# Kernel tuning notes

Hardware: AMD Instinct MI355X
Metric: run time of the kernel (lower is better)

## Reference

```python
import jax, jax.numpy as jnp
import numpy as np

B, S, D = 4, 2048, 1024
E, K, H = 8, 2, 4096


def setup_inputs() -> dict:
    key = jax.random.key(0)
    ks = jax.random.split(key, 8)
    sd = 1.0 / np.sqrt(D)
    sh = 1.0 / np.sqrt(H)
    x = jax.random.normal(ks[0], (B, S, D), dtype=jnp.float32)
    gate_w = jax.random.normal(ks[1], (D, E), dtype=jnp.float32) * sd
    gate_b = jnp.zeros((E,), dtype=jnp.float32)
    w1 = jax.random.normal(ks[2], (E, D, H), dtype=jnp.float32) * sd
    b1 = jnp.zeros((E, H), dtype=jnp.float32)
    w2 = jax.random.normal(ks[3], (E, H, D), dtype=jnp.float32) * sh
    b2 = jnp.zeros((E, D), dtype=jnp.float32)
    return {"x": x, "gate_w": gate_w, "gate_b": gate_b,
            "w1": w1, "b1": b1, "w2": w2, "b2": b2}


def reference(x, gate_w, gate_b, w1, b1, w2, b2):
    # gate logits [B,S,E]
    logits = jnp.einsum('bsd,de->bse', x, gate_w) + gate_b
    # top-k over experts, softmax over the k selected (dim=2), in float32
    weights, selected = jax.lax.top_k(logits, K)            # [B,S,K]
    weights = jax.nn.softmax(weights.astype(jnp.float32), axis=-1).astype(x.dtype)
    out = jnp.zeros_like(x)
    for i in range(E):
        # per-token combine weight for expert i (0 if not routed here)
        w_i = jnp.sum(jnp.where(selected == i, weights, 0.0), axis=-1)  # [B,S]
        h = jax.nn.gelu(jnp.einsum('bsd,dh->bsh', x, w1[i]) + b1[i])    # [B,S,H]
        y = jnp.einsum('bsh,hd->bsd', h, w2[i]) + b2[i]                  # [B,S,D]
        out = out + w_i[..., None] * y
    return out
```

## Files before the change

### kernel.cpp

```cpp
#include <hip/hip_runtime.h>
#include <hip/hip_bf16.h>
#include <stdint.h>

#define T_TOK 8192
#define D_DIM 1024
#define E_NUM 8
#define H_DIM 4096
#define WL_MAX 72

typedef short bf16x8 __attribute__((ext_vector_type(8)));
typedef float f32x4 __attribute__((ext_vector_type(4)));

#define AS1 __attribute__((address_space(1)))
#define AS3 __attribute__((address_space(3)))

__device__ __forceinline__ unsigned short f2b(float f) {
  union { float f; uint32_t u; } v; v.f = f;
  uint32_t r = (v.u + 0x7fffu + ((v.u >> 16) & 1u)) >> 16;
  return (unsigned short)r;
}

__device__ __forceinline__ float gelu_tanh(float x) {
  float u = 0.7978845608028654f * (x + 0.044715f * x * x * x);
  u = fminf(fmaxf(u, -15.f), 15.f);
  float e = __expf(2.f * u);
  float t = (e - 1.f) / (e + 1.f);
  return 0.5f * x * (1.f + t);
}

__device__ __forceinline__ void gload_lds16(const void* g, void* l) {
  __builtin_amdgcn_global_load_lds((const AS1 uint32_t*)g, (AS3 uint32_t*)l, 16, 0, 0);
}

__global__ __launch_bounds__(256) void moe_gate_conv(const float* __restrict__ x,
                                                     const float* __restrict__ gw,
                                                     const float* __restrict__ gb,
                                                     unsigned short* __restrict__ xb,
                                                     int2* __restrict__ sel,
                                                     float2* __restrict__ wts,
                                                     int* __restrict__ meta) {
  int lane = threadIdx.x & 63;
  int t = blockIdx.x * 4 + (threadIdx.x >> 6);
  const float* xr = x + (size_t)t * D_DIM;
  unsigned short* xo = xb + (size_t)t * D_DIM;
  float acc[8];
#pragma unroll
  for (int e = 0; e < 8; e++) acc[e] = 0.f;
#pragma unroll
  for (int i = 0; i < 4; i++) {
    int d0 = lane * 4 + i * 256;
    float4 xv = *(const float4*)(xr + d0);
    ushort4 o;
    o.x = f2b(xv.x); o.y = f2b(xv.y); o.z = f2b(xv.z); o.w = f2b(xv.w);
    *(ushort4*)(xo + d0) = o;
    const float* gp = gw + (size_t)d0 * 8;
    float xs[4] = {xv.x, xv.y, xv.z, xv.w};
#pragma unroll
    for (int j = 0; j < 4; j++) {
#pragma unroll
      for (int e = 0; e < 8; e++) acc[e] += xs[j] * gp[j * 8 + e];
    }
  }
#pragma unroll
  for (int off = 32; off > 0; off >>= 1) {
#pragma unroll
    for (int e = 0; e < 8; e++) acc[e] += __shfl_xor(acc[e], off);
  }
  if (lane == 0) {
    float lg[8];
#pragma unroll
    for (int e = 0; e < 8; e++) lg[e] = acc[e] + gb[e];
    int e0 = 0; float b0 = lg[0];
#pragma unroll
    for (int e = 1; e < 8; e++) if (lg[e] > b0) { b0 = lg[e]; e0 = e; }
    int e1 = -1; float b1v = -1e30f;
#pragma unroll
    for (int e = 0; e < 8; e++) if (e != e0 && lg[e] > b1v) { b1v = lg[e]; e1 = e; }
    float d = __expf(b1v - b0);
    float w0 = 1.f / (1.f + d), w1 = d / (1.f + d);
    sel[t] = make_int2(e0, e1);
    wts[t] = make_float2(w0, w1);
    atomicAdd(&meta[e0], 1);
    atomicAdd(&meta[e1], 1);
  }
}

__global__ __launch_bounds__(256) void moe_transpose(const float* __restrict__ in,
                                                     unsigned short* __restrict__ out,
                                                     int R, int C) {
  int e = blockIdx.z;
  int c0 = blockIdx.x * 64, r0 = blockIdx.y * 64;
  __shared__ float tile[64][65];
  const float* ine = in + (size_t)e * R * C;
  unsigned short* oute = out + (size_t)e * R * C;
  int tr = threadIdx.x >> 2;
  int tc4 = (threadIdx.x & 3) * 16;
#pragma unroll
  for (int p = 0; p < 4; p++) {
    int c = tc4 + p * 4;
    float4 v = *(const float4*)(ine + (size_t)(r0 + tr) * C + c0 + c);
    tile[tr][c] = v.x; tile[tr][c + 1] = v.y; tile[tr][c + 2] = v.z; tile[tr][c + 3] = v.w;
  }
  __syncthreads();
#pragma unroll
  for (int p = 0; p < 4; p++) {
    int rr = tc4 + p * 4;
    ushort4 o;
    o.x = f2b(tile[rr + 0][tr]);
    o.y = f2b(tile[rr + 1][tr]);
    o.z = f2b(tile[rr + 2][tr]);
    o.w = f2b(tile[rr + 3][tr]);
    *(ushort4*)(oute + (size_t)(c0 + tr) * R + r0 + rr) = o;
  }
}

__global__ void moe_scan(int* meta, int2* wl) {
  if (threadIdx.x == 0 && blockIdx.x == 0) {
    int o = 0;
    for (int e = 0; e < 8; e++) { meta[8 + e] = o; meta[20 + e] = o; o += meta[e]; }
    meta[16] = o;
    int w = 0;
    for (int e = 0; e < 8; e++)
      for (int m0 = 0; m0 < meta[e]; m0 += 256) wl[w++] = make_int2(e, m0);
    meta[17] = w;
  }
}

__global__ __launch_bounds__(256) void moe_scatter(const int2* __restrict__ sel,
                                                   int* __restrict__ meta,
                                                   int* __restrict__ token_id,
                                                   int2* __restrict__ pos) {
  int t = blockIdx.x * 256 + threadIdx.x;
  if (t >= T_TOK) return;
  int2 s = sel[t];
  int p0 = atomicAdd(&meta[20 + s.x], 1); token_id[p0] = t;
  int p1 = atomicAdd(&meta[20 + s.y], 1); token_id[p1] = t;
  pos[t] = make_int2(p0, p1);
}

template<int MODE>
__global__ __launch_bounds__(512, 2) void moe_gemm_pipe(
    const unsigned short* __restrict__ Amat,
    const unsigned short* __restrict__ Bmat,
    const float* __restrict__ bias,
    const int* __restrict__ meta,
    const int2* __restrict__ wl,
    const int* __restrict__ token_id,
    unsigned short* __restrict__ hout,
    float* __restrict__ yout) {
  constexpr int KLEN = MODE ? 4096 : 1024;
  constexpr int NK   = MODE ? 64 : 32;
  constexpr int NOUT = MODE ? 1024 : 4096;

  int wi = blockIdx.y;
  if (wi >= meta[17]) return;
  int e = wl[wi].x, m0 = wl[wi].y;
  int seg = meta[8 + e], ne = meta[9 + e] - seg;
  int n0, ks;
  if (MODE) { n0 = (int)(blockIdx.x >> 1) * 256; ks = blockIdx.x & 1; }
  else      { n0 = blockIdx.x * 256; ks = 0; }
  const int kbase = ks * 2048;

  __shared__ unsigned short As[3][8192];
  __shared__ unsigned short Bs[3][8192];

  int tid = threadIdx.x, lane = tid & 63, w = tid >> 6;
  int wm = w >> 2, wn = w & 3;

  const unsigned short* aSrc[2];
  const unsigned short* bSrc[2];
#pragma unroll
  for (int q = 0; q < 2; ++q) {
    int chunk = (w * 2 + q) * 64 + lane;
    int row = chunk >> 2;
    int ko = (chunk & 3) * 8;
    int gi = m0 + row; if (gi >= ne) gi = m0;
    if (MODE) aSrc[q] = Amat + (size_t)(seg + gi) * KLEN + kbase + ko;
    else      aSrc[q] = Amat + (size_t)token_id[seg + gi] * KLEN + ko;
    bSrc[q] = Bmat + (size_t)e * (4096 * 1024) + (size_t)(n0 + row) * KLEN + kbase + ko;
  }

  auto STAGE = [&](int buf, int kt) {
#pragma unroll
    for (int q = 0; q < 2; ++q) {
      gload_lds16(aSrc[q] + kt * 32, &As[buf][(w * 2 + q) * 512]);
      gload_lds16(bSrc[q] + kt * 32, &Bs[buf][(w * 2 + q) * 512]);
    }
  };

  f32x4 acc[8][4] = {};
  const int aoff = (wm * 128 + (lane & 15)) * 32 + (lane >> 4) * 8;
  const int boff = (wn * 64 + (lane & 15)) * 32 + (lane >> 4) * 8;

  STAGE(0, 0); STAGE(1, 1); STAGE(2, 2);

  int t = 0, cur = 0;
#define GSTEP(WAITSTR, DOSTAGE) do { \
    asm volatile("s_waitcnt " WAITSTR ::: "memory"); \
    __builtin_amdgcn_s_barrier(); \
    __builtin_amdgcn_sched_barrier(0); \
    bf16x8 af[8], bv8[4]; \
    _Pragma("unroll") for (int mf = 0; mf < 8; ++mf) af[mf] = *(const bf16x8*)&As[cur][aoff + mf * 512]; \
    _Pragma("unroll") for (int nf = 0; nf < 4; ++nf) bv8[nf] = *(const bf16x8*)&Bs[cur][boff + nf * 512]; \
    asm volatile("s_waitcnt lgkmcnt(0)" ::: "memory"); \
    __builtin_amdgcn_sched_barrier(0); \
    __builtin_amdgcn_s_barrier(); \
    __builtin_amdgcn_sched_barrier(0); \
    if (DOSTAGE) STAGE(cur, t + 3); \
    _Pragma("unroll") for (int mf = 0; mf < 8; ++mf) \
      _Pragma("unroll") for (int nf = 0; nf < 4; ++nf) \
        acc[mf][nf] = __builtin_amdgcn_mfma_f32_16x16x32_bf16(af[mf], bv8[nf], acc[mf][nf], 0, 0, 0); \
    cur = (cur == 2) ? 0 : cur + 1; \
    ++t; \
  } while (0)

  for (int it = 0; it < NK - 3; ++it) GSTEP("vmcnt(8)", true);
  GSTEP("vmcnt(8)", false);
  GSTEP("vmcnt(4)", false);
  GSTEP("vmcnt(0)", false);
#undef GSTEP

  int rb = wm * 128 + (lane >> 4) * 4;
  int cb = n0 + wn * 64 + (lane & 15);
  const float* be = bias + (size_t)e * NOUT + cb;
  float bvv[4];
#pragma unroll
  for (int nf = 0; nf < 4; ++nf) bvv[nf] = (MODE && ks) ? 0.f : be[nf * 16];
#pragma unroll
  for (int mf = 0; mf < 8; ++mf) {
#pragma unroll
    for (int j = 0; j < 4; ++j) {
      int gi = m0 + rb + mf * 16 + j;
      if (gi < ne) {
        if (MODE) {
          float* yrow = yout + (size_t)(seg + gi) * 1024 + cb;
#pragma unroll
          for (int nf = 0; nf < 4; ++nf)
            atomicAdd(&yrow[nf * 16], acc[mf][nf][j] + bvv[nf]);
        } else {
          unsigned short* hrow = hout + (size_t)(seg + gi) * 4096 + cb;
#pragma unroll
          for (int nf = 0; nf < 4; ++nf)
            hrow[nf * 16] = f2b(gelu_tanh(acc[mf][nf][j] + bvv[nf]));
        }
      }
    }
  }
}

__global__ __launch_bounds__(256) void moe_combine(const float* __restrict__ y,
                                                   const int2* __restrict__ pos,
                                                   const float2* __restrict__ wts,
                                                   float* __restrict__ out) {
  int i = blockIdx.x * 256 + threadIdx.x;
  int idx = i * 4;
  int t = idx >> 10, d = idx & 1023;
  int2 p = pos[t];
  float2 w = wts[t];
  float4 a = *(const float4*)(y + (size_t)p.x * D_DIM + d);
  float4 b = *(const float4*)(y + (size_t)p.y * D_DIM + d);
  float4 o;
  o.x = w.x * a.x + w.y * b.x;
  o.y = w.x * a.y + w.y * b.y;
  o.z = w.x * a.z + w.y * b.z;
  o.w = w.x * a.w + w.y * b.w;
  *(float4*)(out + idx) = o;
}

extern "C" void kernel_launch(void* const* d_in, const int* in_sizes, int n_in,
                              void* d_out, int out_size, void* d_ws, size_t ws_size,
                              hipStream_t stream) {
  const float* x      = (const float*)d_in[0];
  const float* gate_w = (const float*)d_in[1];
  const float* gate_b = (const float*)d_in[2];
  const float* w1     = (const float*)d_in[3];
  const float* b1     = (const float*)d_in[4];
  const float* w2     = (const float*)d_in[5];
  const float* b2     = (const float*)d_in[6];
  float* out = (float*)d_out;

  uint8_t* ws = (uint8_t*)d_ws;
  unsigned short* hbuf = (unsigned short*)(ws);
  unsigned short* xb   = (unsigned short*)(ws + 134217728ull);
  unsigned short* w1t  = (unsigned short*)(ws + 150994944ull);
  float*          yb   = (float*)         (ws + 150994944ull);
  unsigned short* w2t  = (unsigned short*)(ws + 218103808ull);
  int*    token_id = (int*)  (ws + 285212672ull);
  int2*   pos      = (int2*) (ws + 285278208ull);
  float2* wts      = (float2*)(ws + 285343744ull);
  int2*   sel      = (int2*) (ws + 285409280ull);
  int*    meta     = (int*)  (ws + 285474816ull);
  int2*   wl       = (int2*) (ws + 285475328ull);

  hipMemsetAsync(meta, 0, 512, stream);

  moe_gate_conv<<<dim3(T_TOK / 4), 256, 0, stream>>>(x, gate_w, gate_b, xb, sel, wts, meta);
  moe_transpose<<<dim3(H_DIM / 64, D_DIM / 64, E_NUM), 256, 0, stream>>>(w1, w1t, D_DIM, H_DIM);
  moe_transpose<<<dim3(D_DIM / 64, H_DIM / 64, E_NUM), 256, 0, stream>>>(w2, w2t, H_DIM, D_DIM);
  moe_scan<<<1, 64, 0, stream>>>(meta, wl);
  moe_scatter<<<dim3(T_TOK / 256), 256, 0, stream>>>(sel, meta, token_id, pos);

  moe_gemm_pipe<0><<<dim3(H_DIM / 256, WL_MAX), 512, 0, stream>>>(
      xb, w1t, b1, meta, wl, token_id, hbuf, nullptr);

  hipMemsetAsync(yb, 0, (size_t)T_TOK * 2 * D_DIM * sizeof(float), stream);

  moe_gemm_pipe<1><<<dim3((D_DIM / 256) * 2, WL_MAX), 512, 0, stream>>>(
      hbuf, w2t, b2, meta, wl, token_id, nullptr, yb);

  moe_combine<<<dim3((T_TOK * D_DIM) / 1024), 256, 0, stream>>>(yb, pos, wts, out);
}
```

Measured before the change: 934.5 us.

## Fuse MoE combine into down-proj epilogue, swizzle LDS, rework GEMM pipeline

The down-projection GEMM now scales its partial results by each token's routing weight and atomically adds them straight into the output. The output is pre-filled with the weighted expert biases, which removes the intermediate y buffer, its memset and the combine kernel. LDS tiles get an XOR swizzle on both the global-to-LDS store mapping and the fragment reads, to reduce bank conflicts. The main loop becomes a single loop with prefetch distance 2 over three buffers and raises wave priority during the MFMA blocks. Atomics now land on token-scattered rows, so contention and access locality may change.

```diff
diff --git a/kernel.cpp b/kernel.cpp
--- a/kernel.cpp
+++ b/kernel.cpp
@@ -127,15 +127,34 @@
 }
 
 __global__ __launch_bounds__(256) void moe_scatter(const int2* __restrict__ sel,
+                                                   const float2* __restrict__ wts,
                                                    int* __restrict__ meta,
                                                    int* __restrict__ token_id,
-                                                   int2* __restrict__ pos) {
+                                                   float* __restrict__ weightv) {
   int t = blockIdx.x * 256 + threadIdx.x;
   if (t >= T_TOK) return;
   int2 s = sel[t];
-  int p0 = atomicAdd(&meta[20 + s.x], 1); token_id[p0] = t;
-  int p1 = atomicAdd(&meta[20 + s.y], 1); token_id[p1] = t;
-  pos[t] = make_int2(p0, p1);
+  float2 w = wts[t];
+  int p0 = atomicAdd(&meta[20 + s.x], 1); token_id[p0] = t; weightv[p0] = w.x;
+  int p1 = atomicAdd(&meta[20 + s.y], 1); token_id[p1] = t; weightv[p1] = w.y;
+}
+
+__global__ __launch_bounds__(256) void moe_outinit(const int2* __restrict__ sel,
+                                                   const float2* __restrict__ wts,
+                                                   const float* __restrict__ b2,
+                                                   float* __restrict__ out) {
+  int t = blockIdx.x;
+  int d = threadIdx.x * 4;
+  int2 s = sel[t];
+  float2 w = wts[t];
+  float4 a = *(const float4*)(b2 + (size_t)s.x * D_DIM + d);
+  float4 b = *(const float4*)(b2 + (size_t)s.y * D_DIM + d);
+  float4 o;
+  o.x = w.x * a.x + w.y * b.x;
+  o.y = w.x * a.y + w.y * b.y;
+  o.z = w.x * a.z + w.y * b.z;
+  o.w = w.x * a.w + w.y * b.w;
+  *(float4*)(out + (size_t)t * D_DIM + d) = o;
 }
 
 template<int MODE>
@@ -146,20 +165,19 @@
     const int* __restrict__ meta,
     const int2* __restrict__ wl,
     const int* __restrict__ token_id,
+    const float* __restrict__ weightv,
     unsigned short* __restrict__ hout,
     float* __restrict__ yout) {
   constexpr int KLEN = MODE ? 4096 : 1024;
   constexpr int NK   = MODE ? 64 : 32;
-  constexpr int NOUT = MODE ? 1024 : 4096;
 
   int wi = blockIdx.y;
   if (wi >= meta[17]) return;
   int e = wl[wi].x, m0 = wl[wi].y;
   int seg = meta[8 + e], ne = meta[9 + e] - seg;
-  int n0, ks;
-  if (MODE) { n0 = (int)(blockIdx.x >> 1) * 256; ks = blockIdx.x & 1; }
-  else      { n0 = blockIdx.x * 256; ks = 0; }
-  const int kbase = ks * 2048;
+  int n0, kbase;
+  if (MODE) { n0 = (int)(blockIdx.x >> 1) * 256; kbase = (int)(blockIdx.x & 1) * 2048; }
+  else      { n0 = blockIdx.x * 256; kbase = 0; }
 
   __shared__ unsigned short As[3][8192];
   __shared__ unsigned short Bs[3][8192];
@@ -167,13 +185,15 @@
   int tid = threadIdx.x, lane = tid & 63, w = tid >> 6;
   int wm = w >> 2, wn = w & 3;
 
+  int binv = (lane & 0x38) | ((lane ^ (lane >> 2)) & 6) | ((lane ^ (lane >> 2) ^ (lane >> 4)) & 1);
+
   const unsigned short* aSrc[2];
   const unsigned short* bSrc[2];
 #pragma unroll
   for (int q = 0; q < 2; ++q) {
-    int chunk = (w * 2 + q) * 64 + lane;
-    int row = chunk >> 2;
-    int ko = (chunk & 3) * 8;
+    int lchunk = ((w * 2 + q) << 6) | binv;
+    int row = lchunk >> 2;
+    int ko = (lchunk & 3) * 8;
     int gi = m0 + row; if (gi >= ne) gi = m0;
     if (MODE) aSrc[q] = Amat + (size_t)(seg + gi) * KLEN + kbase + ko;
     else      aSrc[q] = Amat + (size_t)token_id[seg + gi] * KLEN + ko;
@@ -189,56 +209,65 @@
   };
 
   f32x4 acc[8][4] = {};
-  const int aoff = (wm * 128 + (lane & 15)) * 32 + (lane >> 4) * 8;
-  const int boff = (wn * 64 + (lane & 15)) * 32 + (lane >> 4) * 8;
-
-  STAGE(0, 0); STAGE(1, 1); STAGE(2, 2);
-
-  int t = 0, cur = 0;
-#define GSTEP(WAITSTR, DOSTAGE) do { \
-    asm volatile("s_waitcnt " WAITSTR ::: "memory"); \
-    __builtin_amdgcn_s_barrier(); \
-    __builtin_amdgcn_sched_barrier(0); \
-    bf16x8 af[8], bv8[4]; \
-    _Pragma("unroll") for (int mf = 0; mf < 8; ++mf) af[mf] = *(const bf16x8*)&As[cur][aoff + mf * 512]; \
-    _Pragma("unroll") for (int nf = 0; nf < 4; ++nf) bv8[nf] = *(const bf16x8*)&Bs[cur][boff + nf * 512]; \
-    asm volatile("s_waitcnt lgkmcnt(0)" ::: "memory"); \
-    __builtin_amdgcn_sched_barrier(0); \
-    __builtin_amdgcn_s_barrier(); \
-    __builtin_amdgcn_sched_barrier(0); \
-    if (DOSTAGE) STAGE(cur, t + 3); \
-    _Pragma("unroll") for (int mf = 0; mf < 8; ++mf) \
-      _Pragma("unroll") for (int nf = 0; nf < 4; ++nf) \
-        acc[mf][nf] = __builtin_amdgcn_mfma_f32_16x16x32_bf16(af[mf], bv8[nf], acc[mf][nf], 0, 0, 0); \
-    cur = (cur == 2) ? 0 : cur + 1; \
-    ++t; \
-  } while (0)
-
-  for (int it = 0; it < NK - 3; ++it) GSTEP("vmcnt(8)", true);
-  GSTEP("vmcnt(8)", false);
-  GSTEP("vmcnt(4)", false);
-  GSTEP("vmcnt(0)", false);
-#undef GSTEP
+  const int aoff = (((wm * 128 + (lane & 15)) * 32 + (lane >> 4) * 8)) ^ ((lane & 7) << 3);
+  const int boff = (((wn * 64 + (lane & 15)) * 32 + (lane >> 4) * 8)) ^ ((lane & 7) << 3);
+
+  STAGE(0, 0); STAGE(1, 1);
+
+  int cur = 0, sb = 2;
+  for (int t = 0; t < NK; ++t) {
+    if (t + 1 < NK) { asm volatile("s_waitcnt vmcnt(4)" ::: "memory"); }
+    else            { asm volatile("s_waitcnt vmcnt(0)" ::: "memory"); }
+    __builtin_amdgcn_s_barrier();
+    if (t + 2 < NK) STAGE(sb, t + 2);
+    bf16x8 af[8], bv8[4];
+#pragma unroll
+    for (int mf = 0; mf < 8; ++mf) af[mf] = *(const bf16x8*)&As[cur][aoff + mf * 512];
+#pragma unroll
+    for (int nf = 0; nf < 4; ++nf) bv8[nf] = *(const bf16x8*)&Bs[cur][boff + nf * 512];
+    __builtin_amdgcn_s_setprio(1);
+#pragma unroll
+    for (int mf = 0; mf < 8; ++mf)
+#pragma unroll
+      for (int nf = 0; nf < 4; ++nf)
+        acc[mf][nf] = __builtin_amdgcn_mfma_f32_16x16x32_bf16(af[mf], bv8[nf], acc[mf][nf], 0, 0, 0);
+    __builtin_amdgcn_s_setprio(0);
+    __builtin_amdgcn_sched_barrier(0);
+    cur = (cur == 2) ? 0 : cur + 1;
+    sb  = (sb  == 2) ? 0 : sb  + 1;
+  }
 
   int rb = wm * 128 + (lane >> 4) * 4;
   int cb = n0 + wn * 64 + (lane & 15);
-  const float* be = bias + (size_t)e * NOUT + cb;
-  float bvv[4];
-#pragma unroll
-  for (int nf = 0; nf < 4; ++nf) bvv[nf] = (MODE && ks) ? 0.f : be[nf * 16];
-#pragma unroll
-  for (int mf = 0; mf < 8; ++mf) {
-#pragma unroll
-    for (int j = 0; j < 4; ++j) {
-      int gi = m0 + rb + mf * 16 + j;
-      if (gi < ne) {
-        if (MODE) {
-          float* yrow = yout + (size_t)(seg + gi) * 1024 + cb;
+  if (MODE) {
+#pragma unroll
+    for (int mf = 0; mf < 8; ++mf) {
+#pragma unroll
+      for (int j = 0; j < 4; ++j) {
+        int gi = m0 + rb + mf * 16 + j;
+        if (gi < ne) {
+          int p = seg + gi;
+          int tok = token_id[p];
+          float wt = weightv[p];
+          float* orow = yout + (size_t)tok * D_DIM + cb;
 #pragma unroll
           for (int nf = 0; nf < 4; ++nf)
-            atomicAdd(&yrow[nf * 16], acc[mf][nf][j] + bvv[nf]);
-        } else {
-          unsigned short* hrow = hout + (size_t)(seg + gi) * 4096 + cb;
+            atomicAdd(&orow[nf * 16], wt * acc[mf][nf][j]);
+        }
+      }
+    }
+  } else {
+    const float* be = bias + (size_t)e * H_DIM + cb;
+    float bvv[4];
+#pragma unroll
+    for (int nf = 0; nf < 4; ++nf) bvv[nf] = be[nf * 16];
+#pragma unroll
+    for (int mf = 0; mf < 8; ++mf) {
+#pragma unroll
+      for (int j = 0; j < 4; ++j) {
+        int gi = m0 + rb + mf * 16 + j;
+        if (gi < ne) {
+          unsigned short* hrow = hout + (size_t)(seg + gi) * H_DIM + cb;
 #pragma unroll
           for (int nf = 0; nf < 4; ++nf)
             hrow[nf * 16] = f2b(gelu_tanh(acc[mf][nf][j] + bvv[nf]));
@@ -246,25 +275,6 @@
       }
     }
   }
-}
-
-__global__ __launch_bounds__(256) void moe_combine(const float* __restrict__ y,
-                                                   const int2* __restrict__ pos,
-                                                   const float2* __restrict__ wts,
-                                                   float* __restrict__ out) {
-  int i = blockIdx.x * 256 + threadIdx.x;
-  int idx = i * 4;
-  int t = idx >> 10, d = idx & 1023;
-  int2 p = pos[t];
-  float2 w = wts[t];
-  float4 a = *(const float4*)(y + (size_t)p.x * D_DIM + d);
-  float4 b = *(const float4*)(y + (size_t)p.y * D_DIM + d);
-  float4 o;
-  o.x = w.x * a.x + w.y * b.x;
-  o.y = w.x * a.y + w.y * b.y;
-  o.z = w.x * a.z + w.y * b.z;
-  o.w = w.x * a.w + w.y * b.w;
-  *(float4*)(out + idx) = o;
 }
 
 extern "C" void kernel_launch(void* const* d_in, const int* in_sizes, int n_in,
@@ -283,10 +293,9 @@
   unsigned short* hbuf = (unsigned short*)(ws);
   unsigned short* xb   = (unsigned short*)(ws + 134217728ull);
   unsigned short* w1t  = (unsigned short*)(ws + 150994944ull);
-  float*          yb   = (float*)         (ws + 150994944ull);
   unsigned short* w2t  = (unsigned short*)(ws + 218103808ull);
   int*    token_id = (int*)  (ws + 285212672ull);
-  int2*   pos      = (int2*) (ws + 285278208ull);
+  float*  weightv  = (float*)(ws + 285278208ull);
   float2* wts      = (float2*)(ws + 285343744ull);
   int2*   sel      = (int2*) (ws + 285409280ull);
   int*    meta     = (int*)  (ws + 285474816ull);
@@ -298,15 +307,12 @@
   moe_transpose<<<dim3(H_DIM / 64, D_DIM / 64, E_NUM), 256, 0, stream>>>(w1, w1t, D_DIM, H_DIM);
   moe_transpose<<<dim3(D_DIM / 64, H_DIM / 64, E_NUM), 256, 0, stream>>>(w2, w2t, H_DIM, D_DIM);
   moe_scan<<<1, 64, 0, stream>>>(meta, wl);
-  moe_scatter<<<dim3(T_TOK / 256), 256, 0, stream>>>(sel, meta, token_id, pos);
+  moe_scatter<<<dim3(T_TOK / 256), 256, 0, stream>>>(sel, wts, meta, token_id, weightv);
+  moe_outinit<<<dim3(T_TOK), 256, 0, stream>>>(sel, wts, b2, out);
 
   moe_gemm_pipe<0><<<dim3(H_DIM / 256, WL_MAX), 512, 0, stream>>>(
-      xb, w1t, b1, meta, wl, token_id, hbuf, nullptr);
-
-  hipMemsetAsync(yb, 0, (size_t)T_TOK * 2 * D_DIM * sizeof(float), stream);
+      xb, w1t, b1, meta, wl, token_id, weightv, hbuf, nullptr);
 
   moe_gemm_pipe<1><<<dim3((D_DIM / 256) * 2, WL_MAX), 512, 0, stream>>>(
-      hbuf, w2t, b2, meta, wl, token_id, nullptr, yb);
-
-  moe_combine<<<dim3((T_TOK * D_DIM) / 1024), 256, 0, stream>>>(yb, pos, wts, out);
-}
+      hbuf, w2t, nullptr, meta, wl, token_id, weightv, nullptr, out);
+}
```

Result: slower. 971.7 us (+4.0%).
